# Performance work log

Measured on AMD Instinct MI355X. Metric: run time of the kernel, lower is better.

Reference implementation:

```python
import jax, jax.numpy as jnp
import numpy as np

L, B, D = 512, 32, 256  # seq_len, batch (hardcoded 32 in source), in_size == hidden_size
H = D


def setup_inputs() -> dict:
    key = jax.random.key(0)
    ks = jax.random.split(key, 9)
    s_in = 1.0 / np.sqrt(D)
    s_h = 1.0 / np.sqrt(H)
    return {
        "v": jax.random.normal(ks[0], (L, B, D), jnp.float32),
        "h0": jax.random.normal(ks[1], (B, H), jnp.float32),       # torch.randn h
        "Vvec": jax.random.normal(ks[2], (B, H), jnp.float32),     # torch.randn V (squeezed [B,H,1])
        "Wp": jax.random.normal(ks[3], (H, D), jnp.float32) * s_in,   # nn.Linear(D,H,bias=False).weight
        "Wp_": jax.random.normal(ks[4], (H, D), jnp.float32) * s_in,
        "W_ih": jax.random.normal(ks[5], (3 * H, D), jnp.float32) * s_h,  # GRUCell weight_ih
        "W_hh": jax.random.normal(ks[6], (3 * H, H), jnp.float32) * s_h,
        "b_ih": jax.random.normal(ks[7], (3 * H,), jnp.float32) * s_h,
        "b_hh": jax.random.normal(ks[8], (3 * H,), jnp.float32) * s_h,
    }


def _gru_cell(c, h, W_ih, W_hh, b_ih, b_hh):
    # torch.nn.GRUCell math
    gi = c @ W_ih.T + b_ih   # [B, 3H]
    gh = h @ W_hh.T + b_hh   # [B, 3H]
    i_r, i_z, i_n = jnp.split(gi, 3, axis=1)
    h_r, h_z, h_n = jnp.split(gh, 3, axis=1)
    r = jax.nn.sigmoid(i_r + h_r)
    z = jax.nn.sigmoid(i_z + h_z)
    n = jnp.tanh(i_n + r * h_n)
    return (1.0 - z) * n + z * h


def reference(v, h0, Vvec, Wp, Wp_, W_ih, W_hh, b_ih, b_hh):
    # Hoist the two linear projections out of the scan (they don't depend on h).
    xq = jnp.einsum('lbd,hd->lbh', v, Wp)    # Wp(v[i]) for all i
    xv = jnp.einsum('lbd,hd->lbh', v, Wp_)   # Wp_(v), reused every step

    def step(h, xq_i):
        x = jnp.tanh(xq_i[None, :, :] + xv)          # [L, B, H]
        s = jnp.einsum('lbh,bh->bl', x, Vvec)        # attention scores over L
        a = jax.nn.softmax(s, axis=1)                # [B, L]
        c = jnp.einsum('bl,lbd->bd', a, v)           # context [B, D]
        h_new = _gru_cell(c, h, W_ih, W_hh, b_ih, b_hh)
        return h_new, h_new

    _, hs = jax.lax.scan(step, h0, xq)  # hs: [L, B, H]
    # dropout is identity in eval mode
    return hs
```

## Files before the change

### kernel.cpp

```cpp
#include <hip/hip_runtime.h>
#include <stdint.h>


#define C2    2.8853900817779268f
#define LOG2E 1.4426950408889634f

typedef __fp16 f16x2 __attribute__((ext_vector_type(2)));
typedef __fp16 f16x4_t __attribute__((ext_vector_type(4)));
typedef __fp16 f16x8 __attribute__((ext_vector_type(8)));
typedef float f32x4 __attribute__((ext_vector_type(4)));

static __device__ __forceinline__ float rcp_f(float x)  { return __builtin_amdgcn_rcpf(x); }
static __device__ __forceinline__ float exp2_f(float x) { return __builtin_amdgcn_exp2f(x); }
#if __has_builtin(__builtin_amdgcn_rcph)
static __device__ __forceinline__ __fp16 rcph(__fp16 x) {
  return (__fp16)__builtin_amdgcn_rcph((_Float16)x);
}
#else
static __device__ __forceinline__ __fp16 rcph(__fp16 x) {
  return (__fp16)__builtin_amdgcn_rcpf((float)x);
}
#endif
static __device__ __forceinline__ float dot2f(f16x2 a, f16x2 b, float c) {
  return __builtin_amdgcn_fdot2(a, b, c, false);
}
static __device__ __forceinline__ f16x8 cvt8(float4 a, float4 b) {
  f16x8 f;
  f[0] = (__fp16)a.x; f[1] = (__fp16)a.y; f[2] = (__fp16)a.z; f[3] = (__fp16)a.w;
  f[4] = (__fp16)b.x; f[5] = (__fp16)b.y; f[6] = (__fp16)b.z; f[7] = (__fp16)b.w;
  return f;
}


__global__ __launch_bounds__(256) void proj_k(
    const float* __restrict__ v, const float* __restrict__ Wp,
    const float* __restrict__ Wp_, __fp16* __restrict__ Eq,
    __fp16* __restrict__ Ev)
{
  __shared__ __align__(16) __fp16 As[64][40];
  __shared__ __align__(16) __fp16 Wqs[64][40];
  __shared__ __align__(16) __fp16 Wvs[64][40];
  const int t = threadIdx.x, wave = t >> 6, lane = t & 63;
  const int quad = lane >> 4, col = lane & 15;
  const int n0 = blockIdx.x * 64, m0 = blockIdx.y * 64;
  const int srow = t >> 2, skq = t & 3;

  f32x4 accq[4], accv[4];
#pragma unroll
  for (int nt = 0; nt < 4; ++nt) {
    accq[nt] = (f32x4){0.f, 0.f, 0.f, 0.f};
    accv[nt] = (f32x4){0.f, 0.f, 0.f, 0.f};
  }

  for (int kc = 0; kc < 8; ++kc) {
    const int k0 = kc * 32;
    {
      const float4* ap = (const float4*)&v[(size_t)(m0 + srow) * 256 + k0 + skq * 8];
      *(f16x8*)&As[srow][skq * 8] = cvt8(ap[0], ap[1]);
      const float4* qp = (const float4*)&Wp[(size_t)(n0 + srow) * 256 + k0 + skq * 8];
      *(f16x8*)&Wqs[srow][skq * 8] = cvt8(qp[0], qp[1]);
      const float4* vp = (const float4*)&Wp_[(size_t)(n0 + srow) * 256 + k0 + skq * 8];
      *(f16x8*)&Wvs[srow][skq * 8] = cvt8(vp[0], vp[1]);
    }
    __syncthreads();
    f16x8 a = *(const f16x8*)&As[wave * 16 + col][quad * 8];
#pragma unroll
    for (int nt = 0; nt < 4; ++nt) {
      f16x8 bq = *(const f16x8*)&Wqs[nt * 16 + col][quad * 8];
      f16x8 bv = *(const f16x8*)&Wvs[nt * 16 + col][quad * 8];
      accq[nt] = __builtin_amdgcn_mfma_f32_16x16x32_f16(a, bq, accq[nt], 0, 0, 0);
      accv[nt] = __builtin_amdgcn_mfma_f32_16x16x32_f16(a, bv, accv[nt], 0, 0, 0);
    }
    __syncthreads();
  }

#pragma unroll
  for (int nt = 0; nt < 4; ++nt)
#pragma unroll
    for (int r = 0; r < 4; ++r) {
      size_t m = m0 + wave * 16 + quad * 4 + r;
      size_t n = n0 + nt * 16 + col;
      float eq = C2 * accq[nt][r], ev = C2 * accv[nt][r];
      eq = fminf(fmaxf(eq, -14.f), 15.5f);
      ev = fminf(fmaxf(ev, -14.f), 15.5f);
      Eq[m * 256 + n] = (__fp16)exp2_f(eq);
      Ev[m * 256 + n] = (__fp16)exp2_f(ev);
    }
}

__global__ __launch_bounds__(256) void vt_k(
    const float* __restrict__ v, __fp16* __restrict__ VT)
{
  __shared__ float Ts[32][33];
  const int t = threadIdx.x;
  const int d0 = blockIdx.x * 32, l0 = blockIdx.y * 32, b = blockIdx.z;
  {
    int lrow = t >> 3, dq = t & 7;
    float4 a = *(const float4*)&v[((size_t)(l0 + lrow) * 32 + b) * 256 + d0 + dq * 4];
    Ts[dq * 4 + 0][lrow] = a.x; Ts[dq * 4 + 1][lrow] = a.y;
    Ts[dq * 4 + 2][lrow] = a.z; Ts[dq * 4 + 3][lrow] = a.w;
  }
  __syncthreads();
  {
    int drow = t >> 3, lq = t & 7;
    f16x4_t o;
#pragma unroll
    for (int e = 0; e < 4; ++e) o[e] = (__fp16)Ts[drow][lq * 4 + e];
    *(f16x4_t*)&VT[((size_t)b * 256 + d0 + drow) * 512 + l0 + lq * 4] = o;
  }
}

__global__ __launch_bounds__(256) void score_k(
    const __fp16* __restrict__ Eq, const __fp16* __restrict__ Ev,
    const float* __restrict__ Vvec, float* __restrict__ S)
{
  __shared__ __align__(16) __fp16 Eqs[64][72];
  __shared__ __align__(16) __fp16 Evs[32][72];
  __shared__ __align__(16) __fp16 Vs[256];
  const int t = threadIdx.x;
  const int tx = t & 15, ty = t >> 4;
  const int l0 = blockIdx.x * 32;
  const int i0 = blockIdx.y * 64;
  const int b  = blockIdx.z;

  Vs[t] = (__fp16)(-2.0f * Vvec[b * 256 + t]);
  float acc[4][2] = {};
  const f16x2 one2 = {(__fp16)1.f, (__fp16)1.f};

  for (int st = 0; st < 4; ++st) {
    const int h0 = st * 64;
#pragma unroll
    for (int s = 0; s < 2; ++s) {
      int f = t + s * 256;
      int row = f >> 3, cq = f & 7;
      *(f16x8*)&Eqs[row][cq * 8] =
          *(const f16x8*)&Eq[((size_t)(i0 + row) * 32 + b) * 256 + h0 + cq * 8];
    }
    {
      int row = t >> 3, cq = t & 7;
      *(f16x8*)&Evs[row][cq * 8] =
          *(const f16x8*)&Ev[((size_t)(l0 + row) * 32 + b) * 256 + h0 + cq * 8];
    }
    __syncthreads();

#pragma unroll
    for (int k8 = 0; k8 < 8; ++k8) {
      f16x8 vh8 = *(const f16x8*)&Vs[h0 + k8 * 8];
      f16x8 ev80 = *(const f16x8*)&Evs[tx][k8 * 8];
      f16x8 ev81 = *(const f16x8*)&Evs[tx + 16][k8 * 8];
      f16x8 eq8[4];
#pragma unroll
      for (int r = 0; r < 4; ++r)
        eq8[r] = *(const f16x8*)&Eqs[ty * 4 + r][k8 * 8];
#pragma unroll
      for (int q = 0; q < 4; ++q) {
        f16x2 vh2 = {vh8[q * 2], vh8[q * 2 + 1]};
        f16x2 e0  = {ev80[q * 2], ev80[q * 2 + 1]};
        f16x2 e1  = {ev81[q * 2], ev81[q * 2 + 1]};
#pragma unroll
        for (int r = 0; r < 4; ++r) {
          f16x2 eq2 = {eq8[r][q * 2], eq8[r][q * 2 + 1]};
          f16x2 d0 = eq2 * e0 + one2;
          f16x2 d1 = eq2 * e1 + one2;
          f16x2 r0 = {rcph(d0[0]), rcph(d0[1])};
          f16x2 r1 = {rcph(d1[0]), rcph(d1[1])};
          acc[r][0] = dot2f(vh2, r0, acc[r][0]);
          acc[r][1] = dot2f(vh2, r1, acc[r][1]);
        }
      }
    }
    __syncthreads();
  }

#pragma unroll
  for (int r = 0; r < 4; ++r) {
    float* ps = &S[((size_t)b * 512 + i0 + ty * 4 + r) * 512 + l0];
    ps[tx]      = acc[r][0];
    ps[tx + 16] = acc[r][1];
  }
}

__global__ __launch_bounds__(512) void ctxsm_k(
    const float* __restrict__ S, const __fp16* __restrict__ VT,
    float* __restrict__ C)
{
  __shared__ __align__(16) __fp16 As[64][40];
  __shared__ __align__(16) __fp16 Vs[256][40];
  __shared__ float red[64][8];
  __shared__ float stat_m[64], stat_inv[64];
  const int t = threadIdx.x, wave = t >> 6, lane = t & 63;
  const int quad = lane >> 4, col = lane & 15;
  const int i0 = blockIdx.x * 64, b = blockIdx.y;
  const int mt = wave & 3, nh = wave >> 2;

  {
    const int row = t >> 3, seg = t & 7;
    const float* sp = &S[((size_t)b * 512 + i0 + row) * 512 + seg * 64];
    float m = -1e30f;
#pragma unroll
    for (int u = 0; u < 16; ++u) {
      float4 x = *(const float4*)&sp[u * 4];
      m = fmaxf(m, fmaxf(fmaxf(x.x, x.y), fmaxf(x.z, x.w)));
    }
    red[row][seg] = m;
    __syncthreads();
    if (seg == 0) {
      float mm = red[row][0];
#pragma unroll
      for (int u = 1; u < 8; ++u) mm = fmaxf(mm, red[row][u]);
      stat_m[row] = mm;
    }
    __syncthreads();
    float M = stat_m[row];
    float s = 0.f;
#pragma unroll
    for (int u = 0; u < 16; ++u) {
      float4 x = *(const float4*)&sp[u * 4];
      s += exp2_f(LOG2E * (x.x - M)) + exp2_f(LOG2E * (x.y - M)) +
           exp2_f(LOG2E * (x.z - M)) + exp2_f(LOG2E * (x.w - M));
    }
    red[row][seg] = s;
    __syncthreads();
    if (seg == 0) {
      float ss = red[row][0];
#pragma unroll
      for (int u = 1; u < 8; ++u) ss += red[row][u];
      stat_inv[row] = rcp_f(ss);
    }
    __syncthreads();
  }

  f32x4 acc[8];
#pragma unroll
  for (int n = 0; n < 8; ++n) acc[n] = (f32x4){0.f, 0.f, 0.f, 0.f};

  for (int kc = 0; kc < 16; ++kc) {
    const int l0 = kc * 32;
    {
      int arow = t >> 3, aq = t & 7;
      float M = stat_m[arow], inv = stat_inv[arow];
      float4 x = *(const float4*)&S[((size_t)b * 512 + i0 + arow) * 512 + l0 + aq * 4];
      f16x4_t o;
      o[0] = (__fp16)(exp2_f(LOG2E * (x.x - M)) * inv);
      o[1] = (__fp16)(exp2_f(LOG2E * (x.y - M)) * inv);
      o[2] = (__fp16)(exp2_f(LOG2E * (x.z - M)) * inv);
      o[3] = (__fp16)(exp2_f(LOG2E * (x.w - M)) * inv);
      *(f16x4_t*)&As[arow][aq * 4] = o;
#pragma unroll
      for (int s2 = 0; s2 < 2; ++s2) {
        int f = t + s2 * 512;
        int vrow = f >> 2, vq = f & 3;
        *(f16x8*)&Vs[vrow][vq * 8] =
            *(const f16x8*)&VT[((size_t)b * 256 + vrow) * 512 + l0 + vq * 8];
      }
    }
    __syncthreads();
    f16x8 a = *(const f16x8*)&As[mt * 16 + col][quad * 8];
#pragma unroll
    for (int n = 0; n < 8; ++n) {
      f16x8 vf = *(const f16x8*)&Vs[nh * 128 + n * 16 + col][quad * 8];
      acc[n] = __builtin_amdgcn_mfma_f32_16x16x32_f16(a, vf, acc[n], 0, 0, 0);
    }
    __syncthreads();
  }

#pragma unroll
  for (int n = 0; n < 8; ++n)
#pragma unroll
    for (int r = 0; r < 4; ++r) {
      size_t i = i0 + mt * 16 + quad * 4 + r;
      size_t d = nh * 128 + n * 16 + col;
      C[(i * 32 + b) * 256 + d] = acc[n][r];
    }
}

__global__ __launch_bounds__(256) void gi_k(
    const float* __restrict__ A, const float* __restrict__ W,
    const float* __restrict__ bih, const float* __restrict__ bhh,
    __fp16* __restrict__ G)
{
  __shared__ __align__(16) __fp16 As[64][40];
  __shared__ __align__(16) __fp16 Ws[64][40];
  const int t = threadIdx.x, wave = t >> 6, lane = t & 63;
  const int quad = lane >> 4, col = lane & 15;
  const int n0 = blockIdx.x * 64, m0 = blockIdx.y * 64;
  const int srow = t >> 2, skq = t & 3;

  f32x4 acc[4];
#pragma unroll
  for (int nt = 0; nt < 4; ++nt) acc[nt] = (f32x4){0.f, 0.f, 0.f, 0.f};

  for (int kc = 0; kc < 8; ++kc) {
    const int k0 = kc * 32;
    {
      const float4* ap = (const float4*)&A[(size_t)(m0 + srow) * 256 + k0 + skq * 8];
      *(f16x8*)&As[srow][skq * 8] = cvt8(ap[0], ap[1]);
      const float4* wp = (const float4*)&W[(size_t)(n0 + srow) * 256 + k0 + skq * 8];
      *(f16x8*)&Ws[srow][skq * 8] = cvt8(wp[0], wp[1]);
    }
    __syncthreads();
    f16x8 a = *(const f16x8*)&As[wave * 16 + col][quad * 8];
#pragma unroll
    for (int nt = 0; nt < 4; ++nt) {
      f16x8 b = *(const f16x8*)&Ws[nt * 16 + col][quad * 8];
      acc[nt] = __builtin_amdgcn_mfma_f32_16x16x32_f16(a, b, acc[nt], 0, 0, 0);
    }
    __syncthreads();
  }

#pragma unroll
  for (int nt = 0; nt < 4; ++nt) {
    int n = n0 + nt * 16 + col;
    float bias = bih[n] + (n < 512 ? bhh[n] : 0.f);
#pragma unroll
    for (int r = 0; r < 4; ++r) {
      size_t m = m0 + wave * 16 + quad * 4 + r;
      G[m * 768 + n] = (__fp16)(acc[nt][r] + bias);
    }
  }
}

__global__ __launch_bounds__(512, 1) void gru_k(
    const __fp16* __restrict__ Gi2, const float* __restrict__ Whh,
    const float* __restrict__ bhh, const float* __restrict__ h0,
    float* __restrict__ out)
{
  __shared__ __align__(16) __fp16 hA[2][256];
  const int t = threadIdx.x, wave = t >> 6, lane = t & 63;
  const int quad = lane >> 4, col = lane & 15;
  const int b = blockIdx.x;
  const int jw = wave * 32;
  const int pa = quad >> 1;
  const int ja = jw + pa * 16 + col;
  const bool writer = (quad & 1) == 0;

  f16x8 Bf[2][3][8];
#pragma unroll
  for (int p = 0; p < 2; ++p)
#pragma unroll
    for (int g = 0; g < 3; ++g) {
      const float* wrow = &Whh[(size_t)(g * 256 + jw + p * 16 + col) * 256];
#pragma unroll
      for (int kk = 0; kk < 8; ++kk) {
        const float4* wp = (const float4*)&wrow[kk * 32 + quad * 8];
        Bf[p][g][kk] = cvt8(wp[0], wp[1]);
      }
    }

  const float bn = bhh[512 + ja];
  float hold;
  {
    float h = h0[(size_t)b * 256 + ja];
    hold = h;
    if (writer) hA[0][ja] = (__fp16)h;
  }
  __syncthreads();

  const __fp16* gp = &Gi2[(size_t)b * 768 + ja];
  __fp16 gcur[3];
#pragma unroll
  for (int g = 0; g < 3; ++g) gcur[g] = gp[g * 256];
  const __fp16* gq = gp + 24576;

  float* outp = &out[(size_t)b * 256 + ja];

  f32x4 acc[2][3];
#pragma unroll
  for (int p = 0; p < 2; ++p)
#pragma unroll
    for (int g = 0; g < 3; ++g)
      acc[p][g] = (f32x4){0.f, 0.f, 0.f, 0.f};

  for (int i = 0; i < 512; ++i) {
    __fp16 gnext[3];
    gnext[0] = gq[0];
    gnext[1] = gq[256];
    gnext[2] = gq[512];
    gq += 24576;

#pragma unroll
    for (int p = 0; p < 2; ++p)
#pragma unroll
      for (int g = 0; g < 3; ++g)
        acc[p][g][0] = 0.f;

    const __fp16* hbuf = hA[i & 1];
#pragma unroll
    for (int kk = 0; kk < 8; ++kk) {
      f16x8 a = *(const f16x8*)&hbuf[kk * 32 + quad * 8];
#pragma unroll
      for (int p = 0; p < 2; ++p)
#pragma unroll
        for (int g = 0; g < 3; ++g)
          acc[p][g] = __builtin_amdgcn_mfma_f32_16x16x32_f16(
              a, Bf[p][g][kk], acc[p][g], 0, 0, 0);
    }

    float ar = pa ? acc[1][0][0] : acc[0][0][0];
    float az = pa ? acc[1][1][0] : acc[0][1][0];
    float an = pa ? acc[1][2][0] : acc[0][2][0];
    float rr = rcp_f(1.f + exp2_f(-LOG2E * ((float)gcur[0] + ar)));
    float zz = rcp_f(1.f + exp2_f(-LOG2E * ((float)gcur[1] + az)));
    float na = fmaf(rr, an + bn, (float)gcur[2]);
    float nn = fmaf(-2.f, rcp_f(1.f + exp2_f(C2 * na)), 1.f);
    float h  = fmaf(zz, hold - nn, nn);
    hold = h;

    __fp16* hnext = hA[(i + 1) & 1];
    if (writer) {
      outp[0] = h;
      hnext[ja] = (__fp16)h;
    }
    outp += 8192;

    gcur[0] = gnext[0]; gcur[1] = gnext[1]; gcur[2] = gnext[2];

    asm volatile("s_waitcnt lgkmcnt(0)" ::: "memory");
    __builtin_amdgcn_s_barrier();
    asm volatile("" ::: "memory");
  }
}

extern "C" void kernel_launch(void* const* d_in, const int* in_sizes, int n_in,
                              void* d_out, int out_size, void* d_ws, size_t ws_size,
                              hipStream_t stream)
{
  const float* v   = (const float*)d_in[0];
  const float* h0  = (const float*)d_in[1];
  const float* Vv  = (const float*)d_in[2];
  const float* Wp  = (const float*)d_in[3];
  const float* Wp_ = (const float*)d_in[4];
  const float* Wih = (const float*)d_in[5];
  const float* Whh = (const float*)d_in[6];
  const float* bih = (const float*)d_in[7];
  const float* bhh = (const float*)d_in[8];
  float* out = (float*)d_out;
  float* ws  = (float*)d_ws;

  __fp16* Eq  = (__fp16*)ws;
  __fp16* Ev  = (__fp16*)(ws + 2097152);
  __fp16* VT  = (__fp16*)(ws + 4194304);
  float*  S   = ws + 6291456;
  float*  C   = ws;
  __fp16* Gi2 = (__fp16*)(ws + 6291456);

  proj_k<<<dim3(4, 256), 256, 0, stream>>>(v, Wp, Wp_, Eq, Ev);
  vt_k<<<dim3(8, 16, 32), 256, 0, stream>>>(v, VT);
  score_k<<<dim3(16, 8, 32), 256, 0, stream>>>(Eq, Ev, Vv, S);
  ctxsm_k<<<dim3(8, 32), 512, 0, stream>>>(S, VT, C);
  gi_k<<<dim3(12, 256), 256, 0, stream>>>(C, Wih, bih, bhh, Gi2);
  gru_k<<<32, 512, 0, stream>>>(Gi2, Whh, bhh, h0, out);
}
```

Measured before the change: 882.7 us.

## Replace MFMA recurrent matvec with per-thread dot2 rows split across two halves

The GRU recurrence previously ran a 16x16x32 MFMA per step, where most of each tile was wasted because only one batch row is live. Now each of 512 threads owns one output row. Threads 0-255 compute r and half of n, threads 256-511 compute z and the other half of n, all with fdot2 over register-resident fp16 weights. Partial results are exchanged through shared memory. This adds a second barrier per step and about 192 weight registers per thread, which risks long serial dot chains and register spills.

```diff
diff --git a/kernel.cpp b/kernel.cpp
--- a/kernel.cpp
+++ b/kernel.cpp
@@ -326,95 +326,116 @@
     float* __restrict__ out)
 {
   __shared__ __align__(16) __fp16 hA[2][256];
-  const int t = threadIdx.x, wave = t >> 6, lane = t & 63;
-  const int quad = lane >> 4, col = lane & 15;
+  __shared__ __align__(16) float xbuf[256][2];
+  const int t = threadIdx.x;
+  const bool hlane = t < 256;
+  const int j = hlane ? t : (t - 256);
   const int b = blockIdx.x;
-  const int jw = wave * 32;
-  const int pa = quad >> 1;
-  const int ja = jw + pa * 16 + col;
-  const bool writer = (quad & 1) == 0;
-
-  f16x8 Bf[2][3][8];
-#pragma unroll
-  for (int p = 0; p < 2; ++p)
-#pragma unroll
-    for (int g = 0; g < 3; ++g) {
-      const float* wrow = &Whh[(size_t)(g * 256 + jw + p * 16 + col) * 256];
-#pragma unroll
-      for (int kk = 0; kk < 8; ++kk) {
-        const float4* wp = (const float4*)&wrow[kk * 32 + quad * 8];
-        Bf[p][g][kk] = cvt8(wp[0], wp[1]);
+
+  f16x2 Wr_[128];
+  f16x2 Wn_[64];
+  {
+    const float* prow = &Whh[(size_t)((hlane ? 0 : 256) + j) * 256];
+    const float* nrow = &Whh[(size_t)(512 + j) * 256 + (hlane ? 0 : 128)];
+#pragma unroll
+    for (int u = 0; u < 64; ++u) {
+      float4 x = *(const float4*)&prow[u * 4];
+      Wr_[u * 2 + 0] = (f16x2){(__fp16)x.x, (__fp16)x.y};
+      Wr_[u * 2 + 1] = (f16x2){(__fp16)x.z, (__fp16)x.w};
+    }
+#pragma unroll
+    for (int u = 0; u < 32; ++u) {
+      float4 x = *(const float4*)&nrow[u * 4];
+      Wn_[u * 2 + 0] = (f16x2){(__fp16)x.x, (__fp16)x.y};
+      Wn_[u * 2 + 1] = (f16x2){(__fp16)x.z, (__fp16)x.w};
+    }
+  }
+
+  float hold = 0.f, bn = 0.f;
+  if (hlane) {
+    hold = h0[(size_t)b * 256 + j];
+    bn = bhh[512 + j];
+    hA[0][j] = (__fp16)hold;
+  }
+  __syncthreads();
+
+  const __fp16* gp = &Gi2[(size_t)b * 768 + (hlane ? j : 256 + j)];
+  float g0 = (float)gp[0];
+  float g1 = hlane ? (float)gp[512] : 0.f;
+  const __fp16* gq = gp + 24576;
+
+  float* outp = &out[(size_t)b * 256 + j];
+
+  for (int i = 0; i < 512; ++i) {
+    float n0f = (float)gq[0];
+    float n1f = hlane ? (float)gq[512] : 0.f;
+    gq += 24576;
+
+    const __fp16* hbuf = hA[i & 1];
+    float pa0 = 0.f, pa1 = 0.f, pa2 = 0.f, pa3 = 0.f;
+    float pn0 = 0.f, pn1 = 0.f;
+    if (hlane) {
+#pragma unroll
+      for (int c = 0; c < 32; ++c) {
+        f16x8 hc = *(const f16x8*)&hbuf[c * 8];
+        f16x2 h0c = __builtin_shufflevector(hc, hc, 0, 1);
+        f16x2 h1c = __builtin_shufflevector(hc, hc, 2, 3);
+        f16x2 h2c = __builtin_shufflevector(hc, hc, 4, 5);
+        f16x2 h3c = __builtin_shufflevector(hc, hc, 6, 7);
+        pa0 = dot2f(h0c, Wr_[c * 4 + 0], pa0);
+        pa1 = dot2f(h1c, Wr_[c * 4 + 1], pa1);
+        pa2 = dot2f(h2c, Wr_[c * 4 + 2], pa2);
+        pa3 = dot2f(h3c, Wr_[c * 4 + 3], pa3);
+        if (c < 16) {
+          pn0 = dot2f(h0c, Wn_[c * 4 + 0], pn0);
+          pn1 = dot2f(h1c, Wn_[c * 4 + 1], pn1);
+          pn0 = dot2f(h2c, Wn_[c * 4 + 2], pn0);
+          pn1 = dot2f(h3c, Wn_[c * 4 + 3], pn1);
+        }
       }
-    }
-
-  const float bn = bhh[512 + ja];
-  float hold;
-  {
-    float h = h0[(size_t)b * 256 + ja];
-    hold = h;
-    if (writer) hA[0][ja] = (__fp16)h;
-  }
-  __syncthreads();
-
-  const __fp16* gp = &Gi2[(size_t)b * 768 + ja];
-  __fp16 gcur[3];
-#pragma unroll
-  for (int g = 0; g < 3; ++g) gcur[g] = gp[g * 256];
-  const __fp16* gq = gp + 24576;
-
-  float* outp = &out[(size_t)b * 256 + ja];
-
-  f32x4 acc[2][3];
-#pragma unroll
-  for (int p = 0; p < 2; ++p)
-#pragma unroll
-    for (int g = 0; g < 3; ++g)
-      acc[p][g] = (f32x4){0.f, 0.f, 0.f, 0.f};
-
-  for (int i = 0; i < 512; ++i) {
-    __fp16 gnext[3];
-    gnext[0] = gq[0];
-    gnext[1] = gq[256];
-    gnext[2] = gq[512];
-    gq += 24576;
-
-#pragma unroll
-    for (int p = 0; p < 2; ++p)
-#pragma unroll
-      for (int g = 0; g < 3; ++g)
-        acc[p][g][0] = 0.f;
-
-    const __fp16* hbuf = hA[i & 1];
-#pragma unroll
-    for (int kk = 0; kk < 8; ++kk) {
-      f16x8 a = *(const f16x8*)&hbuf[kk * 32 + quad * 8];
-#pragma unroll
-      for (int p = 0; p < 2; ++p)
-#pragma unroll
-        for (int g = 0; g < 3; ++g)
-          acc[p][g] = __builtin_amdgcn_mfma_f32_16x16x32_f16(
-              a, Bf[p][g][kk], acc[p][g], 0, 0, 0);
-    }
-
-    float ar = pa ? acc[1][0][0] : acc[0][0][0];
-    float az = pa ? acc[1][1][0] : acc[0][1][0];
-    float an = pa ? acc[1][2][0] : acc[0][2][0];
-    float rr = rcp_f(1.f + exp2_f(-LOG2E * ((float)gcur[0] + ar)));
-    float zz = rcp_f(1.f + exp2_f(-LOG2E * ((float)gcur[1] + az)));
-    float na = fmaf(rr, an + bn, (float)gcur[2]);
-    float nn = fmaf(-2.f, rcp_f(1.f + exp2_f(C2 * na)), 1.f);
-    float h  = fmaf(zz, hold - nn, nn);
-    hold = h;
-
-    __fp16* hnext = hA[(i + 1) & 1];
-    if (writer) {
+    } else {
+#pragma unroll
+      for (int c = 0; c < 32; ++c) {
+        f16x8 hc = *(const f16x8*)&hbuf[c * 8];
+        f16x2 h0c = __builtin_shufflevector(hc, hc, 0, 1);
+        f16x2 h1c = __builtin_shufflevector(hc, hc, 2, 3);
+        f16x2 h2c = __builtin_shufflevector(hc, hc, 4, 5);
+        f16x2 h3c = __builtin_shufflevector(hc, hc, 6, 7);
+        pa0 = dot2f(h0c, Wr_[c * 4 + 0], pa0);
+        pa1 = dot2f(h1c, Wr_[c * 4 + 1], pa1);
+        pa2 = dot2f(h2c, Wr_[c * 4 + 2], pa2);
+        pa3 = dot2f(h3c, Wr_[c * 4 + 3], pa3);
+        if (c >= 16) {
+          pn0 = dot2f(h0c, Wn_[(c - 16) * 4 + 0], pn0);
+          pn1 = dot2f(h1c, Wn_[(c - 16) * 4 + 1], pn1);
+          pn0 = dot2f(h2c, Wn_[(c - 16) * 4 + 2], pn0);
+          pn1 = dot2f(h3c, Wn_[(c - 16) * 4 + 3], pn1);
+        }
+      }
+    }
+    float ghp = (pa0 + pa1) + (pa2 + pa3);
+    float pn  = pn0 + pn1;
+    float sig = rcp_f(1.f + exp2_f(-LOG2E * (g0 + ghp)));
+    if (!hlane) {
+      xbuf[j][0] = sig;
+      xbuf[j][1] = pn;
+    }
+    asm volatile("s_waitcnt lgkmcnt(0)" ::: "memory");
+    __builtin_amdgcn_s_barrier();
+    asm volatile("" ::: "memory");
+    if (hlane) {
+      float zz  = xbuf[j][0];
+      float pnz = xbuf[j][1];
+      float ghn = (pn + pnz) + bn;
+      float na  = fmaf(sig, ghn, g1);
+      float nn  = fmaf(-2.f, rcp_f(1.f + exp2_f(C2 * na)), 1.f);
+      float h   = fmaf(zz, hold - nn, nn);
+      hold = h;
       outp[0] = h;
-      hnext[ja] = (__fp16)h;
+      hA[(i + 1) & 1][j] = (__fp16)h;
     }
     outp += 8192;
-
-    gcur[0] = gnext[0]; gcur[1] = gnext[1]; gcur[2] = gnext[2];
-
+    g0 = n0f; g1 = n1f;
     asm volatile("s_waitcnt lgkmcnt(0)" ::: "memory");
     __builtin_amdgcn_s_barrier();
     asm volatile("" ::: "memory");
```

After: 1.190 ms. 34.8% more time.

## Replace MFMA recurrent matvec in GRU kernel with register-resident dot2 matvec

Applied to the files above, without the earlier changes.

Rewrites the sequential GRU recurrence kernel so that each of 1024 threads holds one quarter of a hidden unit's three W_hh rows as packed fp16 in registers. Each thread computes partial dot products with fdot2 against the shared hidden state, and the four partials are reduced with lane shuffles. This replaces the mostly wasted 16x16 MFMA tiles, where only one row of the batch-of-one matvec was used, with plain vector math. The goal is a shorter per-step critical path. The hidden buffer is padded per quarter to limit LDS bank conflicts. The block size doubles, which raises register pressure (96 packed weight registers per thread) and makes the per-step barrier span more waves.

```diff
diff --git a/kernel.cpp b/kernel.cpp
--- a/kernel.cpp
+++ b/kernel.cpp
@@ -320,100 +320,91 @@
   }
 }
 
-__global__ __launch_bounds__(512, 1) void gru_k(
+__global__ __launch_bounds__(1024, 1) void gru_k(
     const __fp16* __restrict__ Gi2, const float* __restrict__ Whh,
     const float* __restrict__ bhh, const float* __restrict__ h0,
     float* __restrict__ out)
 {
-  __shared__ __align__(16) __fp16 hA[2][256];
-  const int t = threadIdx.x, wave = t >> 6, lane = t & 63;
-  const int quad = lane >> 4, col = lane & 15;
+  __shared__ __align__(16) __fp16 hA[2][320];
+  const int t = threadIdx.x;
+  const int j = t >> 2, q = t & 3;
   const int b = blockIdx.x;
-  const int jw = wave * 32;
-  const int pa = quad >> 1;
-  const int ja = jw + pa * 16 + col;
-  const bool writer = (quad & 1) == 0;
-
-  f16x8 Bf[2][3][8];
-#pragma unroll
-  for (int p = 0; p < 2; ++p)
-#pragma unroll
-    for (int g = 0; g < 3; ++g) {
-      const float* wrow = &Whh[(size_t)(g * 256 + jw + p * 16 + col) * 256];
-#pragma unroll
-      for (int kk = 0; kk < 8; ++kk) {
-        const float4* wp = (const float4*)&wrow[kk * 32 + quad * 8];
-        Bf[p][g][kk] = cvt8(wp[0], wp[1]);
-      }
-    }
-
-  const float bn = bhh[512 + ja];
-  float hold;
+  const int k0 = q * 64;
+
+  f16x2 Wr_[32], Wz_[32], Wn_[32];
   {
-    float h = h0[(size_t)b * 256 + ja];
-    hold = h;
-    if (writer) hA[0][ja] = (__fp16)h;
-  }
+    const float* r0 = &Whh[(size_t)(0   + j) * 256 + k0];
+    const float* z0 = &Whh[(size_t)(256 + j) * 256 + k0];
+    const float* n0 = &Whh[(size_t)(512 + j) * 256 + k0];
+#pragma unroll
+    for (int u = 0; u < 16; ++u) {
+      float4 x = *(const float4*)&r0[u * 4];
+      Wr_[u * 2 + 0] = (f16x2){(__fp16)x.x, (__fp16)x.y};
+      Wr_[u * 2 + 1] = (f16x2){(__fp16)x.z, (__fp16)x.w};
+      float4 y = *(const float4*)&z0[u * 4];
+      Wz_[u * 2 + 0] = (f16x2){(__fp16)y.x, (__fp16)y.y};
+      Wz_[u * 2 + 1] = (f16x2){(__fp16)y.z, (__fp16)y.w};
+      float4 z = *(const float4*)&n0[u * 4];
+      Wn_[u * 2 + 0] = (f16x2){(__fp16)z.x, (__fp16)z.y};
+      Wn_[u * 2 + 1] = (f16x2){(__fp16)z.z, (__fp16)z.w};
+    }
+  }
+
+  const float bn = bhh[512 + j];
+  float hold = h0[(size_t)b * 256 + j];
+  const int wslot = (j >> 6) * 80 + (j & 63);
+  if (q == 0) hA[0][wslot] = (__fp16)hold;
   __syncthreads();
 
-  const __fp16* gp = &Gi2[(size_t)b * 768 + ja];
-  __fp16 gcur[3];
-#pragma unroll
-  for (int g = 0; g < 3; ++g) gcur[g] = gp[g * 256];
+  const __fp16* gp = &Gi2[(size_t)b * 768 + j];
+  float gr = (float)gp[0], gz = (float)gp[256], gn = (float)gp[512];
   const __fp16* gq = gp + 24576;
 
-  float* outp = &out[(size_t)b * 256 + ja];
-
-  f32x4 acc[2][3];
-#pragma unroll
-  for (int p = 0; p < 2; ++p)
-#pragma unroll
-    for (int g = 0; g < 3; ++g)
-      acc[p][g] = (f32x4){0.f, 0.f, 0.f, 0.f};
+  float* outp = &out[(size_t)b * 256 + j];
 
   for (int i = 0; i < 512; ++i) {
-    __fp16 gnext[3];
-    gnext[0] = gq[0];
-    gnext[1] = gq[256];
-    gnext[2] = gq[512];
+    float nr = (float)gq[0], nz = (float)gq[256], nn2 = (float)gq[512];
     gq += 24576;
 
-#pragma unroll
-    for (int p = 0; p < 2; ++p)
-#pragma unroll
-      for (int g = 0; g < 3; ++g)
-        acc[p][g][0] = 0.f;
-
-    const __fp16* hbuf = hA[i & 1];
-#pragma unroll
-    for (int kk = 0; kk < 8; ++kk) {
-      f16x8 a = *(const f16x8*)&hbuf[kk * 32 + quad * 8];
-#pragma unroll
-      for (int p = 0; p < 2; ++p)
-#pragma unroll
-        for (int g = 0; g < 3; ++g)
-          acc[p][g] = __builtin_amdgcn_mfma_f32_16x16x32_f16(
-              a, Bf[p][g][kk], acc[p][g], 0, 0, 0);
-    }
-
-    float ar = pa ? acc[1][0][0] : acc[0][0][0];
-    float az = pa ? acc[1][1][0] : acc[0][1][0];
-    float an = pa ? acc[1][2][0] : acc[0][2][0];
-    float rr = rcp_f(1.f + exp2_f(-LOG2E * ((float)gcur[0] + ar)));
-    float zz = rcp_f(1.f + exp2_f(-LOG2E * ((float)gcur[1] + az)));
-    float na = fmaf(rr, an + bn, (float)gcur[2]);
+    const __fp16* hb = &hA[i & 1][q * 80];
+    float ar0 = 0.f, ar1 = 0.f, az0 = 0.f, az1 = 0.f, an0 = 0.f, an1 = 0.f;
+#pragma unroll
+    for (int c = 0; c < 8; ++c) {
+      f16x8 hc = *(const f16x8*)&hb[c * 8];
+      f16x2 h0c = __builtin_shufflevector(hc, hc, 0, 1);
+      f16x2 h1c = __builtin_shufflevector(hc, hc, 2, 3);
+      f16x2 h2c = __builtin_shufflevector(hc, hc, 4, 5);
+      f16x2 h3c = __builtin_shufflevector(hc, hc, 6, 7);
+      ar0 = dot2f(h0c, Wr_[c * 4 + 0], ar0);
+      ar1 = dot2f(h1c, Wr_[c * 4 + 1], ar1);
+      ar0 = dot2f(h2c, Wr_[c * 4 + 2], ar0);
+      ar1 = dot2f(h3c, Wr_[c * 4 + 3], ar1);
+      az0 = dot2f(h0c, Wz_[c * 4 + 0], az0);
+      az1 = dot2f(h1c, Wz_[c * 4 + 1], az1);
+      az0 = dot2f(h2c, Wz_[c * 4 + 2], az0);
+      az1 = dot2f(h3c, Wz_[c * 4 + 3], az1);
+      an0 = dot2f(h0c, Wn_[c * 4 + 0], an0);
+      an1 = dot2f(h1c, Wn_[c * 4 + 1], an1);
+      an0 = dot2f(h2c, Wn_[c * 4 + 2], an0);
+      an1 = dot2f(h3c, Wn_[c * 4 + 3], an1);
+    }
+    float ar = ar0 + ar1, az = az0 + az1, an = an0 + an1;
+    ar += __shfl_xor(ar, 1); ar += __shfl_xor(ar, 2);
+    az += __shfl_xor(az, 1); az += __shfl_xor(az, 2);
+    an += __shfl_xor(an, 1); an += __shfl_xor(an, 2);
+
+    float rr = rcp_f(1.f + exp2_f(-LOG2E * (gr + ar)));
+    float zz = rcp_f(1.f + exp2_f(-LOG2E * (gz + az)));
+    float na = fmaf(rr, an + bn, gn);
     float nn = fmaf(-2.f, rcp_f(1.f + exp2_f(C2 * na)), 1.f);
     float h  = fmaf(zz, hold - nn, nn);
     hold = h;
-
-    __fp16* hnext = hA[(i + 1) & 1];
-    if (writer) {
+    if (q == 0) {
       outp[0] = h;
-      hnext[ja] = (__fp16)h;
+      hA[(i + 1) & 1][wslot] = (__fp16)h;
     }
     outp += 8192;
-
-    gcur[0] = gnext[0]; gcur[1] = gnext[1]; gcur[2] = gnext[2];
+    gr = nr; gz = nz; gn = nn2;
 
     asm volatile("s_waitcnt lgkmcnt(0)" ::: "memory");
     __builtin_amdgcn_s_barrier();
@@ -449,5 +440,5 @@
   score_k<<<dim3(16, 8, 32), 256, 0, stream>>>(Eq, Ev, Vv, S);
   ctxsm_k<<<dim3(8, 32), 512, 0, stream>>>(S, VT, C);
   gi_k<<<dim3(12, 256), 256, 0, stream>>>(C, Wih, bih, bhh, Gi2);
-  gru_k<<<32, 512, 0, stream>>>(Gi2, Whh, bhh, h0, out);
-}
+  gru_k<<<32, 1024, 0, stream>>>(Gi2, Whh, bhh, h0, out);
+}
```

New measurement: 1.042 ms. +18.1%, slower.
